# Optimization experiments

Hardware: AMD Instinct MI355X
Metric: run time of the kernel (lower is better)

Reference implementation:

```python
import jax, jax.numpy as jnp
import numpy as np

C = 128   # d_pair, fixed by the fp8 tri-mul kernel assert
H = 128   # d_hidden


def layer_norm(x, w, b, eps=1e-5):
    m = jnp.mean(x, axis=-1, keepdims=True)
    v = jnp.mean(jnp.square(x - m), axis=-1, keepdims=True)
    return (x - m) * jax.lax.rsqrt(v + eps) * w + b


def setup_inputs() -> dict:
    key = jax.random.key(0)
    ks = jax.random.split(key, 12)
    B, N = 1, 512
    s_in = 1.0 / np.sqrt(C)
    s_h = 1.0 / np.sqrt(H)
    return {
        "z": jax.random.normal(ks[0], (B, N, N, C), jnp.float32),
        "mask": jnp.ones((B, N, N), jnp.float32),
        "ln_in_w": jnp.ones((C,), jnp.float32),
        "ln_in_b": jnp.zeros((C,), jnp.float32),
        "w_ap": jax.random.normal(ks[1], (C, H), jnp.float32) * s_in,
        "b_ap": jnp.zeros((H,), jnp.float32),
        "w_ag": jax.random.normal(ks[2], (C, H), jnp.float32) * s_in,
        "b_ag": jnp.zeros((H,), jnp.float32),
        "w_bp": jax.random.normal(ks[3], (C, H), jnp.float32) * s_in,
        "b_bp": jnp.zeros((H,), jnp.float32),
        "w_bg": jax.random.normal(ks[4], (C, H), jnp.float32) * s_in,
        "b_bg": jnp.zeros((H,), jnp.float32),
        "ln_out_w": jnp.ones((H,), jnp.float32),
        "ln_out_b": jnp.zeros((H,), jnp.float32),
        "w_o": jax.random.normal(ks[5], (H, C), jnp.float32) * s_h,
        "b_o": jnp.zeros((C,), jnp.float32),
        "w_g": jax.random.normal(ks[6], (C, C), jnp.float32) * s_in,
        "b_g": jnp.zeros((C,), jnp.float32),
    }


def reference(z, mask, ln_in_w, ln_in_b, w_ap, b_ap, w_ag, b_ag,
              w_bp, b_bp, w_bg, b_bg, ln_out_w, ln_out_b, w_o, b_o, w_g, b_g):
    # Triangular multiplicative update (outgoing), gated projections.
    z_ln = layer_norm(z, ln_in_w, ln_in_b)                      # [B,N,N,C]
    m = mask[..., None]                                         # [B,N,N,1]
    a = m * jax.nn.sigmoid(z_ln @ w_ag + b_ag) * (z_ln @ w_ap + b_ap)
    b = m * jax.nn.sigmoid(z_ln @ w_bg + b_bg) * (z_ln @ w_bp + b_bp)
    # outgoing: x[b,i,j,c] = sum_k a[b,i,k,c] * b[b,j,k,c]
    x = jnp.einsum("bikc,bjkc->bijc", a, b)                     # [B,N,N,H]
    x = layer_norm(x, ln_out_w, ln_out_b)
    g = jax.nn.sigmoid(z_ln @ w_g + b_g)                        # output gate
    return g * (x @ w_o + b_o)
```

## Files before the change

kernel.cpp:

```cpp
#include <hip/hip_runtime.h>
#include <hip/hip_bf16.h>
#include <stdint.h>

#define NDIM 512
#define NN (NDIM*NDIM)
#define CDIM 128
#define LDSP 136

typedef __attribute__((ext_vector_type(8))) short short8;
typedef __attribute__((ext_vector_type(4))) short short4v;
typedef __attribute__((ext_vector_type(4))) float f32x4;
typedef __attribute__((ext_vector_type(8))) _Float16 half8;
typedef unsigned long long ull;

__device__ __forceinline__ unsigned short f2h(float f) {
    union { _Float16 h; unsigned short u; } v;
    v.h = (_Float16)f;
    return v.u;
}
__device__ __forceinline__ float h2f(unsigned short u) {
    union { _Float16 h; unsigned short u; } v;
    v.u = u;
    return (float)v.h;
}
__device__ __forceinline__ f32x4 mfma16(short8 a, short8 b, f32x4 c) {
    return __builtin_amdgcn_mfma_f32_16x16x32_f16(
        __builtin_bit_cast(half8, a), __builtin_bit_cast(half8, b), c, 0, 0, 0);
}
__device__ __forceinline__ void gl_lds16(const void* g, void* l) {
    __builtin_amdgcn_global_load_lds((const __attribute__((address_space(1))) void*)g,
                                     (__attribute__((address_space(3))) void*)l,
                                     16, 0, 0);
}

__global__ void k0_prep(const float* __restrict__ w_ag, const float* __restrict__ w_ap,
                        const float* __restrict__ w_bg, const float* __restrict__ w_bp,
                        const float* __restrict__ w_g,  const float* __restrict__ w_o,
                        unsigned short* __restrict__ Wfrag, unsigned short* __restrict__ Wo_t)
{
    int idx = blockIdx.x * 256 + threadIdx.x;
    if (idx < 10240) {
        int lane = idx & 63;
        int n  = (idx >> 6) & 3;
        int kk = (idx >> 8) & 3;
        int h  = (idx >> 10) & 1;
        int s  = idx >> 11;
        const float* w = (s==0) ? w_ag : (s==1) ? w_ap : (s==2) ? w_bg : (s==3) ? w_bp : w_g;
        int col = h*64 + n*16 + (lane & 15);
        int k0  = kk*32 + (lane >> 4)*8;
        short8 pk;
        #pragma unroll
        for (int e = 0; e < 8; e++)
            pk[e] = (short)f2h(w[(k0 + e)*128 + col]);
        *(short8*)(Wfrag + (size_t)idx*8) = pk;
    } else if (idx < 10240 + 16384) {
        int i2 = idx - 10240;
        int cc = i2 >> 7, hh = i2 & 127;
        Wo_t[i2] = f2h(w_o[hh*128 + cc]);
    }
}

__global__ __launch_bounds__(512, 2) void k1_proj(
    const float* __restrict__ z, const float* __restrict__ mask,
    const float* __restrict__ lnw, const float* __restrict__ lnb,
    const unsigned short* __restrict__ Wfrag,
    const float* __restrict__ b_ag, const float* __restrict__ b_ap,
    const float* __restrict__ b_bg, const float* __restrict__ b_bp,
    const float* __restrict__ b_g,
    unsigned short* __restrict__ a_t, unsigned short* __restrict__ b_t,
    unsigned short* __restrict__ g_out)
{
    __shared__ unsigned short zb[128*LDSP];
    __shared__ float mask_s[128];
    __shared__ float lnw_s[128];
    __shared__ float lnb_s[128];
    __shared__ float bias_s[640];

    const int t = threadIdx.x;
    const int pos0 = blockIdx.x * 128;
    const int row4 = t >> 2, q = t & 3;
    const int wave = t >> 6, lane = t & 63;
    const int wl = wave & 3, wg = wave >> 2;
    const int lr = lane & 15, lh = lane >> 4;

    if (t < 128) {
        lnw_s[t] = lnw[t];
        lnb_s[t] = lnb[t];
        mask_s[t] = mask[pos0 + t];
    }
    for (int i = t; i < 640; i += 512) {
        int s = i >> 7, c = i & 127;
        const float* bp = (s==0) ? b_ag : (s==1) ? b_ap : (s==2) ? b_bg : (s==3) ? b_bp : b_g;
        bias_s[i] = bp[c];
    }

    float v[32];
    float s0 = 0.f, s1 = 0.f;
    {
        const float* zr = z + (size_t)(pos0 + row4) * CDIM + q * 32;
        #pragma unroll
        for (int i = 0; i < 8; i++) {
            float4 qv = *(const float4*)(zr + i*4);
            v[i*4+0] = qv.x; v[i*4+1] = qv.y; v[i*4+2] = qv.z; v[i*4+3] = qv.w;
        }
        #pragma unroll
        for (int i = 0; i < 32; i++) { s0 += v[i]; s1 += v[i]*v[i]; }
        s0 += __shfl_xor(s0, 1);
        s1 += __shfl_xor(s1, 1);
        s0 += __shfl_xor(s0, 2);
        s1 += __shfl_xor(s1, 2);
    }
    __syncthreads();
    {
        float m  = s0 * (1.f/128.f);
        float va = s1 * (1.f/128.f) - m*m;
        float rs = rsqrtf(va + 1e-5f);
        #pragma unroll
        for (int i = 0; i < 4; i++) {
            short8 pk;
            #pragma unroll
            for (int j = 0; j < 8; j++) {
                int c = q*32 + i*8 + j;
                pk[j] = (short)f2h((v[i*8+j]-m)*rs*lnw_s[c] + lnb_s[c]);
            }
            *(short8*)&zb[row4*LDSP + q*32 + i*8] = pk;
        }
    }
    __syncthreads();

    const int rowA0 = (wl*32 + lr)*LDSP;
    const int rowA1 = (wl*32 + 16 + lr)*LDSP;
    const unsigned short* wfl = Wfrag + (size_t)lane*8;

    auto gemmh = [&](int s, int h, f32x4 (&acc)[2][4]) {
        const unsigned short* wf = wfl + (size_t)(s*2 + h)*8192;
        #pragma unroll
        for (int m = 0; m < 2; m++)
            #pragma unroll
            for (int n = 0; n < 4; n++) { f32x4 zz = {0.f,0.f,0.f,0.f}; acc[m][n] = zz; }
        #pragma unroll
        for (int st = 0; st < 2; st++) {
            short8 wbuf[8];
            #pragma unroll
            for (int i = 0; i < 8; i++)
                wbuf[i] = *(const short8*)(wf + (st*8 + i)*512);
            #pragma unroll
            for (int k2 = 0; k2 < 2; k2++) {
                const int kk = st*2 + k2;
                const int k0 = kk*32 + lh*8;
                short8 af0 = *(const short8*)&zb[rowA0 + k0];
                short8 af1 = *(const short8*)&zb[rowA1 + k0];
                #pragma unroll
                for (int n = 0; n < 4; n++) {
                    acc[0][n] = mfma16(af0, wbuf[k2*4 + n], acc[0][n]);
                    acc[1][n] = mfma16(af1, wbuf[k2*4 + n], acc[1][n]);
                }
            }
        }
    };

    auto pair_half = [&](int sG, int sP, int h, unsigned short* dstg) {
        f32x4 G[2][4], P[2][4];
        gemmh(sG, h, G);
        gemmh(sP, h, P);
        const int odd = lh & 1;
        const int base = wl*32 + lh*4 + (odd ? 12 : 0);
        #pragma unroll
        for (int n = 0; n < 4; n++) {
            int col = h*64 + n*16 + lr;
            float bgv = bias_s[sG*128 + col];
            float bpv = bias_s[sP*128 + col];
            union { short4v v; ull u; } p0, p1;
            #pragma unroll
            for (int r = 0; r < 4; r++) {
                float g0 = 1.f / (1.f + __expf(-(G[0][n][r] + bgv)));
                p0.v[r] = (short)f2h(mask_s[wl*32 + lh*4 + r] * g0 * (P[0][n][r] + bpv));
                float g1 = 1.f / (1.f + __expf(-(G[1][n][r] + bgv)));
                p1.v[r] = (short)f2h(mask_s[wl*32 + 16 + lh*4 + r] * g1 * (P[1][n][r] + bpv));
            }
            ull r0 = __shfl_xor(p0.u, 16);
            ull r1 = __shfl_xor(p1.u, 16);
            union { ull u[2]; short8 v; } outv;
            outv.u[0] = odd ? r1 : p0.u;
            outv.u[1] = odd ? p1.u : r0;
            *(short8*)(dstg + (size_t)col*NN + pos0 + base) = outv.v;
        }
    };

    if (wg == 0) {
        pair_half(0, 1, 0, a_t);
        pair_half(0, 1, 1, a_t);
    } else {
        pair_half(2, 3, 0, b_t);
        pair_half(2, 3, 1, b_t);
    }

    f32x4 G[2][4];
    gemmh(4, wg, G);
    __syncthreads();
    #pragma unroll
    for (int m = 0; m < 2; m++) {
        int rb = wl*32 + m*16 + lh*4;
        #pragma unroll
        for (int n = 0; n < 4; n++) {
            int c0 = wg*64 + n*16 + lr;
            float b0 = bias_s[512 + c0];
            #pragma unroll
            for (int r = 0; r < 4; r++)
                zb[(rb + r)*LDSP + c0] = f2h(1.f / (1.f + __expf(-(G[m][n][r] + b0))));
        }
    }
    __syncthreads();
    {
        const unsigned short* src = zb + row4*LDSP + q*32;
        unsigned short* dst = g_out + (size_t)(pos0 + row4)*CDIM + q*32;
        #pragma unroll
        for (int i = 0; i < 4; i++)
            *(short8*)(dst + i*8) = *(const short8*)(src + i*8);
    }
}

__global__ __launch_bounds__(256, 2) void k2_einsum(
    const unsigned short* __restrict__ a_t,
    const unsigned short* __restrict__ b_t,
    unsigned short* __restrict__ x_t)
{
    __shared__ unsigned short As[128*64];
    __shared__ unsigned short Bs[128*64];

    const int c  = blockIdx.y;
    const int ti = (blockIdx.x >> 2) * 128;
    const int tj = (blockIdx.x & 3) * 128;
    const int t = threadIdx.x;
    const int wave = t >> 6, lane = t & 63;
    const int lr = lane & 15, lh = lane >> 4;
    const int wm = wave >> 1, wn = wave & 1;

    const unsigned short* Ag = a_t + (size_t)c*NN + (size_t)ti*NDIM;
    const unsigned short* Bg = b_t + (size_t)c*NN + (size_t)tj*NDIM;

    const int srow = wave*32 + (lane >> 3);
    const int scol = (lane & 7) * 8;

    f32x4 acc[4][4] = {};

    for (int k0 = 0; k0 < NDIM; k0 += 64) {
        __syncthreads();
        #pragma unroll
        for (int it = 0; it < 4; it++) {
            int r = srow + it*8;
            gl_lds16(Ag + (size_t)r*NDIM + k0 + scol, (void*)(As + (wave*32 + it*8)*64));
            gl_lds16(Bg + (size_t)r*NDIM + k0 + scol, (void*)(Bs + (wave*32 + it*8)*64));
        }
        asm volatile("s_waitcnt vmcnt(0)" ::: "memory");
        __syncthreads();
        #pragma unroll
        for (int kk = 0; kk < 2; kk++) {
            const int kof = kk*32 + lh*8;
            short8 af[4], bfr[4];
            #pragma unroll
            for (int m = 0; m < 4; m++)
                af[m] = *(const short8*)&As[(wm*64 + m*16 + lr)*64 + kof];
            #pragma unroll
            for (int n = 0; n < 4; n++)
                bfr[n] = *(const short8*)&Bs[(wn*64 + n*16 + lr)*64 + kof];
            #pragma unroll
            for (int m = 0; m < 4; m++)
                #pragma unroll
                for (int n = 0; n < 4; n++)
                    acc[m][n] = mfma16(af[m], bfr[n], acc[m][n]);
        }
    }

    #pragma unroll
    for (int m = 0; m < 4; m++) {
        int row = ti + wm*64 + m*16 + lh*4;
        #pragma unroll
        for (int n = 0; n < 4; n++) {
            int col = tj + wn*64 + n*16 + lr;
            unsigned short* dst = x_t + (size_t)c*NN + (size_t)row*NDIM + col;
            #pragma unroll
            for (int r = 0; r < 4; r++)
                dst[(size_t)r*NDIM] = f2h(acc[m][n][r]);
        }
    }
}

__global__ __launch_bounds__(256, 2) void k3_out(
    const unsigned short* __restrict__ x_t,
    const unsigned short* __restrict__ g_in,
    const unsigned short* __restrict__ Wo_t,
    const float* __restrict__ lnw, const float* __restrict__ lnb,
    const float* __restrict__ b_o,
    float* __restrict__ out)
{
    __shared__ unsigned short xb[128*LDSP];
    __shared__ unsigned short zl[128*LDSP];
    __shared__ float lnw_s[128];
    __shared__ float lnb_s[128];
    __shared__ float bo_s[128];

    const int t = threadIdx.x;
    const int pos0 = blockIdx.x * 128;
    const int tid2 = t >> 1, half = t & 1;
    const int wave = t >> 6, lane = t & 63;
    const int lr = lane & 15, lh = lane >> 4;

    if (t < 128) { lnw_s[t] = lnw[t]; lnb_s[t] = lnb[t]; bo_s[t] = b_o[t]; }

    {
        const unsigned short* src = x_t + (size_t)tid2*NN + pos0 + half*64;
        unsigned short* dst = xb + tid2*LDSP + half*64;
        #pragma unroll
        for (int i = 0; i < 8; i++)
            *(short8*)(dst + i*8) = *(const short8*)(src + i*8);
    }
    __syncthreads();

    {
        float v[64];
        float s0 = 0.f, s1 = 0.f;
        #pragma unroll
        for (int i = 0; i < 64; i++) {
            float x = h2f(xb[(half*64 + i)*LDSP + tid2]);
            v[i] = x; s0 += x; s1 += x*x;
        }
        s0 += __shfl_xor(s0, 1);
        s1 += __shfl_xor(s1, 1);
        float m  = s0 * (1.f/128.f);
        float va = s1 * (1.f/128.f) - m*m;
        float rs = rsqrtf(va + 1e-5f);
        #pragma unroll
        for (int i = 0; i < 64; i++) {
            int cc = half*64 + i;
            zl[tid2*LDSP + cc] = f2h((v[i]-m)*rs*lnw_s[cc] + lnb_s[cc]);
        }
    }
    __syncthreads();

    {
        const unsigned short* src = Wo_t + ((size_t)tid2*128 + half*64);
        unsigned short* dst = xb + tid2*LDSP + half*64;
        #pragma unroll
        for (int i = 0; i < 8; i++)
            *(short8*)(dst + i*8) = *(const short8*)(src + i*8);
    }
    __syncthreads();

    f32x4 acc[2][8];
    #pragma unroll
    for (int m = 0; m < 2; m++)
        #pragma unroll
        for (int n = 0; n < 8; n++) { f32x4 zz = {0.f,0.f,0.f,0.f}; acc[m][n] = zz; }

    #pragma unroll
    for (int kk = 0; kk < 4; kk++) {
        const int k0 = kk*32 + lh*8;
        short8 af0 = *(const short8*)&zl[(wave*32 + lr)*LDSP + k0];
        short8 af1 = *(const short8*)&zl[(wave*32 + 16 + lr)*LDSP + k0];
        #pragma unroll
        for (int n = 0; n < 8; n++) {
            short8 bf = *(const short8*)&xb[(n*16 + lr)*LDSP + k0];
            acc[0][n] = mfma16(af0, bf, acc[0][n]);
            acc[1][n] = mfma16(af1, bf, acc[1][n]);
        }
    }
    __syncthreads();

    {
        const unsigned short* src = g_in + (size_t)(pos0 + tid2)*CDIM + half*64;
        unsigned short* dst = zl + tid2*LDSP + half*64;
        #pragma unroll
        for (int i = 0; i < 8; i++)
            *(short8*)(dst + i*8) = *(const short8*)(src + i*8);
    }
    __syncthreads();

    #pragma unroll
    for (int m = 0; m < 2; m++) {
        int rb = wave*32 + m*16 + lh*4;
        #pragma unroll
        for (int n = 0; n < 8; n++) {
            int col = n*16 + lr;
            float bo = bo_s[col];
            #pragma unroll
            for (int r = 0; r < 4; r++) {
                int row = rb + r;
                float gv = h2f(zl[row*LDSP + col]);
                out[(size_t)(pos0 + row)*CDIM + col] = gv * (acc[m][n][r] + bo);
            }
        }
    }
}

extern "C" void kernel_launch(void* const* d_in, const int* in_sizes, int n_in,
                              void* d_out, int out_size, void* d_ws, size_t ws_size,
                              hipStream_t stream) {
    const float* z        = (const float*)d_in[0];
    const float* mask     = (const float*)d_in[1];
    const float* ln_in_w  = (const float*)d_in[2];
    const float* ln_in_b  = (const float*)d_in[3];
    const float* w_ap     = (const float*)d_in[4];
    const float* b_ap     = (const float*)d_in[5];
    const float* w_ag     = (const float*)d_in[6];
    const float* b_ag     = (const float*)d_in[7];
    const float* w_bp     = (const float*)d_in[8];
    const float* b_bp     = (const float*)d_in[9];
    const float* w_bg     = (const float*)d_in[10];
    const float* b_bg     = (const float*)d_in[11];
    const float* ln_out_w = (const float*)d_in[12];
    const float* ln_out_b = (const float*)d_in[13];
    const float* w_o      = (const float*)d_in[14];
    const float* b_o      = (const float*)d_in[15];
    const float* w_g      = (const float*)d_in[16];
    const float* b_g      = (const float*)d_in[17];

    char* ws = (char*)d_ws;
    const size_t BUF = (size_t)NN * 128 * 2;
    unsigned short* a_t   = (unsigned short*)(ws);
    unsigned short* b_t   = (unsigned short*)(ws + BUF);
    unsigned short* g_b   = (unsigned short*)(ws + 2*BUF);
    unsigned short* x_t   = (unsigned short*)(ws + 3*BUF);
    unsigned short* Wfrag = (unsigned short*)(ws + 4*BUF);
    unsigned short* Wo_t  = (unsigned short*)(ws + 4*BUF + (size_t)10240*8*2);

    k0_prep<<<104, 256, 0, stream>>>(w_ag, w_ap, w_bg, w_bp, w_g, w_o, Wfrag, Wo_t);
    k1_proj<<<NN/128, 512, 0, stream>>>(z, mask, ln_in_w, ln_in_b, Wfrag,
                                        b_ag, b_ap, b_bg, b_bp, b_g, a_t, b_t, g_b);
    k2_einsum<<<dim3(16, 128), 256, 0, stream>>>(a_t, b_t, x_t);
    k3_out<<<NN/128, 256, 0, stream>>>(x_t, g_b, Wo_t, ln_out_w, ln_out_b, b_o,
                                       (float*)d_out);
}
```

Baseline: 304.6 us.

## Move output gate GEMM from projection kernel into output kernel via stored LN(z)

The kernel that projects z now stores the fp16 layer-normed z instead of computing the sigmoid output gate. The gate GEMM and its sigmoid move into the output kernel, which reloads LN(z) into shared memory and runs a second MFMA pass against the gate weights. The projection kernel also shrinks to 64-row tiles with 256 threads. The intent is to shorten the projection kernel and move the gate work to the output stage, at the cost of more registers and MFMA work in the output kernel.

Result: faster. 285.5 us (-6.3%).

```diff
diff --git a/kernel.cpp b/kernel.cpp
--- a/kernel.cpp
+++ b/kernel.cpp
@@ -60,37 +60,36 @@
     }
 }
 
-__global__ __launch_bounds__(512, 2) void k1_proj(
+__global__ __launch_bounds__(256, 2) void k1_proj(
     const float* __restrict__ z, const float* __restrict__ mask,
     const float* __restrict__ lnw, const float* __restrict__ lnb,
     const unsigned short* __restrict__ Wfrag,
     const float* __restrict__ b_ag, const float* __restrict__ b_ap,
     const float* __restrict__ b_bg, const float* __restrict__ b_bp,
-    const float* __restrict__ b_g,
     unsigned short* __restrict__ a_t, unsigned short* __restrict__ b_t,
-    unsigned short* __restrict__ g_out)
+    unsigned short* __restrict__ zln)
 {
-    __shared__ unsigned short zb[128*LDSP];
-    __shared__ float mask_s[128];
+    __shared__ unsigned short zb[64*LDSP];
+    __shared__ float mask_s[64];
     __shared__ float lnw_s[128];
     __shared__ float lnb_s[128];
-    __shared__ float bias_s[640];
+    __shared__ float bias_s[512];
 
     const int t = threadIdx.x;
-    const int pos0 = blockIdx.x * 128;
+    const int pos0 = blockIdx.x * 64;
     const int row4 = t >> 2, q = t & 3;
     const int wave = t >> 6, lane = t & 63;
-    const int wl = wave & 3, wg = wave >> 2;
+    const int wl = wave & 1, wg = wave >> 1;
     const int lr = lane & 15, lh = lane >> 4;
 
     if (t < 128) {
         lnw_s[t] = lnw[t];
         lnb_s[t] = lnb[t];
-        mask_s[t] = mask[pos0 + t];
-    }
-    for (int i = t; i < 640; i += 512) {
+    }
+    if (t < 64) mask_s[t] = mask[pos0 + t];
+    for (int i = t; i < 512; i += 256) {
         int s = i >> 7, c = i & 127;
-        const float* bp = (s==0) ? b_ag : (s==1) ? b_ap : (s==2) ? b_bg : (s==3) ? b_bp : b_g;
+        const float* bp = (s==0) ? b_ag : (s==1) ? b_ap : (s==2) ? b_bg : b_bp;
         bias_s[i] = bp[c];
     }
 
@@ -115,6 +114,7 @@
         float m  = s0 * (1.f/128.f);
         float va = s1 * (1.f/128.f) - m*m;
         float rs = rsqrtf(va + 1e-5f);
+        unsigned short* zo = zln + (size_t)(pos0 + row4)*CDIM + q*32;
         #pragma unroll
         for (int i = 0; i < 4; i++) {
             short8 pk;
@@ -124,6 +124,7 @@
                 pk[j] = (short)f2h((v[i*8+j]-m)*rs*lnw_s[c] + lnb_s[c]);
             }
             *(short8*)&zb[row4*LDSP + q*32 + i*8] = pk;
+            *(short8*)(zo + i*8) = pk;
         }
     }
     __syncthreads();
@@ -194,30 +195,6 @@
         pair_half(2, 3, 0, b_t);
         pair_half(2, 3, 1, b_t);
     }
-
-    f32x4 G[2][4];
-    gemmh(4, wg, G);
-    __syncthreads();
-    #pragma unroll
-    for (int m = 0; m < 2; m++) {
-        int rb = wl*32 + m*16 + lh*4;
-        #pragma unroll
-        for (int n = 0; n < 4; n++) {
-            int c0 = wg*64 + n*16 + lr;
-            float b0 = bias_s[512 + c0];
-            #pragma unroll
-            for (int r = 0; r < 4; r++)
-                zb[(rb + r)*LDSP + c0] = f2h(1.f / (1.f + __expf(-(G[m][n][r] + b0))));
-        }
-    }
-    __syncthreads();
-    {
-        const unsigned short* src = zb + row4*LDSP + q*32;
-        unsigned short* dst = g_out + (size_t)(pos0 + row4)*CDIM + q*32;
-        #pragma unroll
-        for (int i = 0; i < 4; i++)
-            *(short8*)(dst + i*8) = *(const short8*)(src + i*8);
-    }
 }
 
 __global__ __launch_bounds__(256, 2) void k2_einsum(
@@ -288,10 +265,11 @@
 
 __global__ __launch_bounds__(256, 2) void k3_out(
     const unsigned short* __restrict__ x_t,
-    const unsigned short* __restrict__ g_in,
+    const unsigned short* __restrict__ zln,
+    const unsigned short* __restrict__ Wfrag,
     const unsigned short* __restrict__ Wo_t,
     const float* __restrict__ lnw, const float* __restrict__ lnb,
-    const float* __restrict__ b_o,
+    const float* __restrict__ b_o, const float* __restrict__ b_g,
     float* __restrict__ out)
 {
     __shared__ unsigned short xb[128*LDSP];
@@ -299,6 +277,7 @@
     __shared__ float lnw_s[128];
     __shared__ float lnb_s[128];
     __shared__ float bo_s[128];
+    __shared__ float bg_s[128];
 
     const int t = threadIdx.x;
     const int pos0 = blockIdx.x * 128;
@@ -306,7 +285,10 @@
     const int wave = t >> 6, lane = t & 63;
     const int lr = lane & 15, lh = lane >> 4;
 
-    if (t < 128) { lnw_s[t] = lnw[t]; lnb_s[t] = lnb[t]; bo_s[t] = b_o[t]; }
+    if (t < 128) {
+        lnw_s[t] = lnw[t]; lnb_s[t] = lnb[t];
+        bo_s[t] = b_o[t];  bg_s[t] = b_g[t];
+    }
 
     {
         const unsigned short* src = x_t + (size_t)tid2*NN + pos0 + half*64;
@@ -347,34 +329,66 @@
     }
     __syncthreads();
 
-    f32x4 acc[2][8];
+    const int rowA0 = (wave*32 + lr)*LDSP;
+    const int rowA1 = (wave*32 + 16 + lr)*LDSP;
+
+    f32x4 acc1[2][8];
     #pragma unroll
     for (int m = 0; m < 2; m++)
         #pragma unroll
-        for (int n = 0; n < 8; n++) { f32x4 zz = {0.f,0.f,0.f,0.f}; acc[m][n] = zz; }
-
+        for (int n = 0; n < 8; n++) { f32x4 zz = {0.f,0.f,0.f,0.f}; acc1[m][n] = zz; }
     #pragma unroll
     for (int kk = 0; kk < 4; kk++) {
         const int k0 = kk*32 + lh*8;
-        short8 af0 = *(const short8*)&zl[(wave*32 + lr)*LDSP + k0];
-        short8 af1 = *(const short8*)&zl[(wave*32 + 16 + lr)*LDSP + k0];
+        short8 af0 = *(const short8*)&zl[rowA0 + k0];
+        short8 af1 = *(const short8*)&zl[rowA1 + k0];
         #pragma unroll
         for (int n = 0; n < 8; n++) {
             short8 bf = *(const short8*)&xb[(n*16 + lr)*LDSP + k0];
-            acc[0][n] = mfma16(af0, bf, acc[0][n]);
-            acc[1][n] = mfma16(af1, bf, acc[1][n]);
-        }
-    }
-    __syncthreads();
-
-    {
-        const unsigned short* src = g_in + (size_t)(pos0 + tid2)*CDIM + half*64;
+            acc1[0][n] = mfma16(af0, bf, acc1[0][n]);
+            acc1[1][n] = mfma16(af1, bf, acc1[1][n]);
+        }
+    }
+    __syncthreads();
+
+    {
+        const unsigned short* src = zln + (size_t)(pos0 + tid2)*CDIM + half*64;
         unsigned short* dst = zl + tid2*LDSP + half*64;
         #pragma unroll
         for (int i = 0; i < 8; i++)
             *(short8*)(dst + i*8) = *(const short8*)(src + i*8);
     }
     __syncthreads();
+
+    f32x4 acc2[2][8];
+    #pragma unroll
+    for (int m = 0; m < 2; m++)
+        #pragma unroll
+        for (int n = 0; n < 8; n++) { f32x4 zz = {0.f,0.f,0.f,0.f}; acc2[m][n] = zz; }
+    const unsigned short* wfl = Wfrag + (size_t)lane*8;
+    #pragma unroll
+    for (int h = 0; h < 2; h++) {
+        const unsigned short* wf = wfl + (size_t)(8 + h)*8192;
+        #pragma unroll
+        for (int st = 0; st < 2; st++) {
+            short8 wbuf[8];
+            #pragma unroll
+            for (int i = 0; i < 8; i++)
+                wbuf[i] = *(const short8*)(wf + (st*8 + i)*512);
+            #pragma unroll
+            for (int k2 = 0; k2 < 2; k2++) {
+                const int kk = st*2 + k2;
+                const int k0 = kk*32 + lh*8;
+                short8 af0 = *(const short8*)&zl[rowA0 + k0];
+                short8 af1 = *(const short8*)&zl[rowA1 + k0];
+                #pragma unroll
+                for (int n = 0; n < 4; n++) {
+                    acc2[0][h*4+n] = mfma16(af0, wbuf[k2*4 + n], acc2[0][h*4+n]);
+                    acc2[1][h*4+n] = mfma16(af1, wbuf[k2*4 + n], acc2[1][h*4+n]);
+                }
+            }
+        }
+    }
 
     #pragma unroll
     for (int m = 0; m < 2; m++) {
@@ -383,11 +397,11 @@
         for (int n = 0; n < 8; n++) {
             int col = n*16 + lr;
             float bo = bo_s[col];
+            float bg = bg_s[col];
             #pragma unroll
             for (int r = 0; r < 4; r++) {
-                int row = rb + r;
-                float gv = h2f(zl[row*LDSP + col]);
-                out[(size_t)(pos0 + row)*CDIM + col] = gv * (acc[m][n][r] + bo);
+                float gv = 1.f / (1.f + __expf(-(acc2[m][n][r] + bg)));
+                out[(size_t)(pos0 + rb + r)*CDIM + col] = gv * (acc1[m][n][r] + bo);
             }
         }
     }
@@ -419,15 +433,15 @@
     const size_t BUF = (size_t)NN * 128 * 2;
     unsigned short* a_t   = (unsigned short*)(ws);
     unsigned short* b_t   = (unsigned short*)(ws + BUF);
-    unsigned short* g_b   = (unsigned short*)(ws + 2*BUF);
+    unsigned short* zln   = (unsigned short*)(ws + 2*BUF);
     unsigned short* x_t   = (unsigned short*)(ws + 3*BUF);
     unsigned short* Wfrag = (unsigned short*)(ws + 4*BUF);
     unsigned short* Wo_t  = (unsigned short*)(ws + 4*BUF + (size_t)10240*8*2);
 
     k0_prep<<<104, 256, 0, stream>>>(w_ag, w_ap, w_bg, w_bp, w_g, w_o, Wfrag, Wo_t);
-    k1_proj<<<NN/128, 512, 0, stream>>>(z, mask, ln_in_w, ln_in_b, Wfrag,
-                                        b_ag, b_ap, b_bg, b_bp, b_g, a_t, b_t, g_b);
+    k1_proj<<<NN/64, 256, 0, stream>>>(z, mask, ln_in_w, ln_in_b, Wfrag,
+                                       b_ag, b_ap, b_bg, b_bp, a_t, b_t, zln);
     k2_einsum<<<dim3(16, 128), 256, 0, stream>>>(a_t, b_t, x_t);
-    k3_out<<<NN/128, 256, 0, stream>>>(x_t, g_b, Wo_t, ln_out_w, ln_out_b, b_o,
-                                       (float*)d_out);
-}
+    k3_out<<<NN/128, 256, 0, stream>>>(x_t, zln, Wfrag, Wo_t, ln_out_w, ln_out_b,
+                                       b_o, b_g, (float*)d_out);
+}
```
